# Kernel optimization log

Measured on AMD Instinct MI355X. Metric: run time of the kernel, lower is better.

Reference implementation:

```python
import jax, jax.numpy as jnp
import numpy as np

B, T, D_MODEL, N_HEAD, D_C = 2, 2048, 2048, 16, 512
D_HEAD = D_MODEL // N_HEAD          # 128
D_ROPE = D_C // N_HEAD              # 32 (rope projections are split into heads too)


def setup_inputs() -> dict:
    key = jax.random.key(0)
    ks = jax.random.split(key, 16)
    s = 0.02
    # weights stored as [in, out] (transpose of torch Linear.weight)
    return {
        "x":     jax.random.normal(ks[0], (B, T, D_MODEL), jnp.float32),
        "W_DKV": jax.random.normal(ks[1], (D_MODEL, D_C), jnp.float32) * s,
        "b_DKV": jnp.zeros((D_C,), jnp.float32),
        "W_UK":  jax.random.normal(ks[2], (D_C, D_MODEL), jnp.float32) * s,
        "b_UK":  jnp.zeros((D_MODEL,), jnp.float32),
        "W_UV":  jax.random.normal(ks[3], (D_C, D_MODEL), jnp.float32) * s,
        "b_UV":  jnp.zeros((D_MODEL,), jnp.float32),
        "W_DQ":  jax.random.normal(ks[4], (D_MODEL, D_C), jnp.float32) * s,
        "b_DQ":  jnp.zeros((D_C,), jnp.float32),
        "W_UQ":  jax.random.normal(ks[5], (D_C, D_MODEL), jnp.float32) * s,
        "b_UQ":  jnp.zeros((D_MODEL,), jnp.float32),
        "W_QR":  jax.random.normal(ks[6], (D_C, D_C), jnp.float32) * s,
        "b_QR":  jnp.zeros((D_C,), jnp.float32),
        "W_KR":  jax.random.normal(ks[7], (D_MODEL, D_C), jnp.float32) * s,
        "b_KR":  jnp.zeros((D_C,), jnp.float32),
    }


def _rope(x):
    # x: [B, H, T, d]; matches torch RoPE: split-even/odd then concat halves
    t, d = x.shape[2], x.shape[-1]
    freqs = 10000.0 ** (-(jnp.arange(0, d, 2, dtype=jnp.float32) / d))  # [d/2]
    theta = jnp.arange(t, dtype=jnp.float32)[:, None] * freqs[None, :]  # [T, d/2]
    cos, sin = jnp.cos(theta), jnp.sin(theta)
    x1, x2 = x[..., ::2], x[..., 1::2]
    return jnp.concatenate([x1 * cos - x2 * sin, x1 * sin + x2 * cos], axis=-1)


def _heads(x):
    b, t, _ = x.shape
    return x.reshape(b, t, N_HEAD, -1).transpose(0, 2, 1, 3)  # [B,H,T,dh]


def reference(x, W_DKV, b_DKV, W_UK, b_UK, W_UV, b_UV, W_DQ, b_DQ,
              W_UQ, b_UQ, W_QR, b_QR, W_KR, b_KR):
    b, t, _ = x.shape
    c_kv = x @ W_DKV + b_DKV                 # [B,T,d_c]
    k_content = _heads(c_kv @ W_UK + b_UK)   # [B,H,T,d_head]
    v = _heads(c_kv @ W_UV + b_UV)           # [B,H,T,d_head]
    c_q = x @ W_DQ + b_DQ
    q_content = _heads(c_q @ W_UQ + b_UQ)    # [B,H,T,d_head]
    q_rope = _rope(_heads(c_q @ W_QR + b_QR))  # [B,H,T,d_rope]
    k_rope = _rope(_heads(x @ W_KR + b_KR))    # [B,H,T,d_rope]
    Q = jnp.concatenate([q_content, q_rope], axis=-1)  # [B,H,T,d_head+d_rope]
    K = jnp.concatenate([k_content, k_rope], axis=-1)
    scale = 1.0 / jnp.sqrt(jnp.float32(Q.shape[-1]))
    scores = jnp.einsum("bhqd,bhkd->bhqk", Q, K) * scale
    probs = jax.nn.softmax(scores, axis=-1)
    out = jnp.einsum("bhqk,bhkd->bhqd", probs, v)
    return out.transpose(0, 2, 1, 3).reshape(b, t, -1)
```

## Files before the change

### kernel.cpp

```cpp
#include <hip/hip_runtime.h>
#include <hip/hip_bf16.h>
#include <cstdint>
#include <cstddef>

typedef __attribute__((ext_vector_type(8)))  short bf16x8;
typedef __attribute__((ext_vector_type(4)))  float f32x4;
typedef __attribute__((ext_vector_type(16))) float f32x16;
typedef __attribute__((ext_vector_type(4)))  int   i32x4;

#define DEVINL __device__ __forceinline__

#define ATT_SCALE 0.07905694150420949f
#define QSCALE    (0.07905694150420949f * 1.4426950408889634f)

DEVINL unsigned short f2bf(float f) {
  unsigned int u = __float_as_uint(f);
  u += 0x7fff + ((u >> 16) & 1);
  return (unsigned short)(u >> 16);
}

DEVINL int cvtpk(float lo, float hi) {
  int r;
  asm("v_cvt_pk_bf16_f32 %0, %1, %2" : "=v"(r) : "v"(lo), "v"(hi));
  return r;
}

DEVINL void stage16(const unsigned short* __restrict__ g, unsigned short* lds_u, int lane) {
  (void)lane;
  __builtin_amdgcn_global_load_lds((const __attribute__((address_space(1))) void*)g,
                                   (__attribute__((address_space(3))) void*)lds_u, 16, 0, 0);
}

__global__ void k_cvt_x(const float* __restrict__ x, unsigned short* __restrict__ o, int n) {
  int i = (blockIdx.x * blockDim.x + threadIdx.x) * 4;
  if (i >= n) return;
  float4 v = *reinterpret_cast<const float4*>(x + i);
  ushort4 r;
  r.x = f2bf(v.x); r.y = f2bf(v.y); r.z = f2bf(v.z); r.w = f2bf(v.w);
  *reinterpret_cast<ushort4*>(o + i) = r;
}

struct TwArgs { const float* W[7]; unsigned short* D[7]; };
__global__ void k_tw_all(TwArgs a) {
  __shared__ float t[32][33];
  const int bid = blockIdx.x;
  int w, K, N, bx, by;
  if (bid < 3072)      { w = bid >> 10; int r = bid & 1023; K = 2048; N = 512;  bx = r & 15; by = r >> 4; }
  else if (bid < 6144) { int r = bid - 3072; w = 3 + (r >> 10); r &= 1023; K = 512; N = 2048; bx = r & 63; by = r >> 6; }
  else                 { int r = bid - 6144; w = 6; K = 512; N = 512; bx = r & 15; by = r >> 4; }
  const float* W = a.W[w];
  unsigned short* D = a.D[w];
  const int n0 = bx * 32, k0 = by * 32;
  const int tx = threadIdx.x, ty = threadIdx.y;
#pragma unroll
  for (int j = 0; j < 4; j++)
    t[ty + j * 8][tx] = W[(size_t)(k0 + ty + j * 8) * N + n0 + tx];
  __syncthreads();
#pragma unroll
  for (int j = 0; j < 4; j++)
    D[(size_t)(n0 + ty + j * 8) * K + k0 + tx] = f2bf(t[tx][ty + j * 8]);
}

DEVINL size_t koff(int bh, int t, int d) {
  const int it = t >> 6, t6 = t & 63;
  const int kvt = t6 >> 5, lanelo = t6 & 31;
  const int ks = d >> 4, hi = (d >> 3) & 1, e = d & 7;
  return ((size_t)bh * 32 + it) * 10240 + (size_t)(kvt * 10 + ks) * 512 + (hi * 32 + lanelo) * 8 + e;
}
DEVINL size_t voff(int bh, int t, int dv) {
  const int it = t >> 6, t6 = t & 63;
  const int ks = t6 >> 4, hi = (t6 >> 3) & 1, e = t6 & 7;
  const int dvt = dv >> 5, lanelo = dv & 31;
  return ((size_t)bh * 32 + it) * 8192 + (size_t)(dvt * 4 + ks) * 512 + (hi * 32 + lanelo) * 8 + e;
}

template <int MODE>
__global__ __launch_bounds__(256) void k_gemm(const unsigned short* __restrict__ A,
                                              const unsigned short* __restrict__ BT,
                                              const float* __restrict__ bias0,
                                              const float* __restrict__ bias1,
                                              const float* __restrict__ bias2,
                                              void* __restrict__ o0, void* __restrict__ o1,
                                              void* __restrict__ o2, int K) {
  __shared__ unsigned short sA[128 * 64];
  __shared__ unsigned short sB[128 * 64];
  const int tid = threadIdx.x;
  const int lane = tid & 63, wid = tid >> 6;
  const int wr = wid >> 1, wc = wid & 1;
  const int row0 = blockIdx.y * 128, col0 = blockIdx.x * 128;
  const int lc = lane & 15, lg = lane >> 4;
  const int srow = lane >> 3, scol = (lane & 7) * 8;

  f32x4 acc[4][4];
#pragma unroll
  for (int m = 0; m < 4; m++)
#pragma unroll
    for (int n = 0; n < 4; n++) acc[m][n] = f32x4{0.f, 0.f, 0.f, 0.f};

  for (int k0 = 0; k0 < K; k0 += 64) {
#pragma unroll
    for (int i = 0; i < 4; i++) {
      const int chunk = wid * 4 + i;
      const int r = chunk * 8 + srow;
      stage16(A + (size_t)(row0 + r) * K + k0 + scol, sA + chunk * 512, lane);
      stage16(BT + (size_t)(col0 + r) * K + k0 + scol, sB + chunk * 512, lane);
    }
    asm volatile("s_waitcnt vmcnt(0)" ::: "memory");
    __syncthreads();
#pragma unroll
    for (int ks = 0; ks < 2; ks++) {
      bf16x8 af[4], bfr[4];
#pragma unroll
      for (int m = 0; m < 4; m++)
        af[m] = *reinterpret_cast<const bf16x8*>(sA + (wr * 64 + m * 16 + lc) * 64 + ks * 32 + lg * 8);
#pragma unroll
      for (int n = 0; n < 4; n++)
        bfr[n] = *reinterpret_cast<const bf16x8*>(sB + (wc * 64 + n * 16 + lc) * 64 + ks * 32 + lg * 8);
#pragma unroll
      for (int m = 0; m < 4; m++)
#pragma unroll
        for (int n = 0; n < 4; n++)
          acc[m][n] = __builtin_amdgcn_mfma_f32_16x16x32_bf16(af[m], bfr[n], acc[m][n], 0, 0, 0);
    }
    __syncthreads();
  }

  const int lr = lg * 4;
#pragma unroll
  for (int m = 0; m < 4; m++)
#pragma unroll
    for (int n = 0; n < 4; n++) {
      const int col = col0 + wc * 64 + n * 16 + lc;
      float bv;
      if constexpr (MODE == 10)
        bv = (col < 512) ? bias0[col] : (col < 1024) ? bias1[col - 512] : bias2[col - 1024];
      else
        bv = (col < 2048) ? bias0[col] : bias1[col - 2048];
#pragma unroll
      for (int r = 0; r < 4; r++) {
        const int row = row0 + wr * 64 + m * 16 + lr + r;
        const float v = acc[m][n][r] + bv;
        const int b = row >> 11, t = row & 2047;
        if constexpr (MODE == 10) {
          if (col < 512)        ((unsigned short*)o0)[(size_t)row * 512 + col] = f2bf(v);
          else if (col < 1024)  ((unsigned short*)o1)[(size_t)row * 512 + col - 512] = f2bf(v);
          else                  ((float*)o2)[(size_t)row * 512 + col - 1024] = v;
        } else if constexpr (MODE == 11) {
          if (col < 2048) {
            const int h = col >> 7, d = col & 127;
            ((unsigned short*)o0)[koff(b * 16 + h, t, d)] = f2bf(v);
          } else {
            const int c = col - 2048, h = c >> 7, dv = c & 127;
            ((unsigned short*)o1)[voff(b * 16 + h, t, dv)] = f2bf(v);
          }
        } else {
          if (col < 2048) {
            const int h = col >> 7, d = col & 127;
            ((unsigned short*)o0)[((size_t)(b * 16 + h) * 2048 + t) * 160 + d] = f2bf(v * QSCALE);
          } else {
            ((float*)o1)[(size_t)row * 512 + col - 2048] = v;
          }
        }
      }
    }
}

__global__ void k_rope(const float* __restrict__ qpre, const float* __restrict__ kpre,
                       unsigned short* __restrict__ Qb, unsigned short* __restrict__ Kf) {
  const int idx = blockIdx.x * blockDim.x + threadIdx.x;
  const int which = idx >> 20;
  const int e = idx & 1048575;
  const int i = e & 15, h = (e >> 4) & 15, row = e >> 8;
  const int t = row & 2047, b = row >> 11;
  const float* pre = which ? kpre : qpre;
  const float x1 = pre[(size_t)row * 512 + h * 32 + 2 * i];
  const float x2 = pre[(size_t)row * 512 + h * 32 + 2 * i + 1];
  const float f = exp2f(-(float)i * (13.287712379549449f / 16.f));
  const float th = (float)t * f;
  float sv, cv;
  sincosf(th, &sv, &cv);
  const float o1 = x1 * cv - x2 * sv, o2 = x1 * sv + x2 * cv;
  if (which == 0) {
    const size_t base = ((size_t)(b * 16 + h) * 2048 + t) * 160 + 128;
    Qb[base + i]      = f2bf(o1 * QSCALE);
    Qb[base + 16 + i] = f2bf(o2 * QSCALE);
  } else {
    Kf[koff(b * 16 + h, t, 128 + i)] = f2bf(o1);
    Kf[koff(b * 16 + h, t, 144 + i)] = f2bf(o2);
  }
}

__global__ __launch_bounds__(256, 2) void k_attn(const unsigned short* __restrict__ Qb,
                                                 const unsigned short* __restrict__ Kf,
                                                 const unsigned short* __restrict__ Vf,
                                                 float* __restrict__ out) {
  __shared__ unsigned short sK[2][10240];
  const int lane = threadIdx.x & 63, wid = threadIdx.x >> 6;
  const int lanelo = lane & 31, hi = lane >> 5;

  const int L = blockIdx.x;
  const int xcd = L & 7, w = L >> 3;
  const int bh = xcd * 4 + (w & 3);
  const int qblk = w >> 2;
  const int b = bh >> 4, h = bh & 15;
  const int q0 = qblk * 128 + wid * 32;

  const unsigned short* Qh = Qb + (size_t)bh * 2048 * 160;
  const unsigned short* Kh = Kf + (size_t)bh * 32 * 10240;
  const unsigned short* Vh = Vf + (size_t)bh * 32 * 8192;

  bf16x8 qf[10];
#pragma unroll
  for (int ks = 0; ks < 10; ks++)
    qf[ks] = *reinterpret_cast<const bf16x8*>(Qh + (size_t)(q0 + lanelo) * 160 + ks * 16 + hi * 8);

#pragma unroll
  for (int i = 0; i < 5; i++) {
    const int chunk = wid * 5 + i;
    stage16(Kh + (size_t)chunk * 512 + lane * 8, &sK[0][0] + chunk * 512, lane);
  }

  f32x16 o[4] = {};
  float mrun = -1e30f, lrun = 0.f;

  asm volatile("s_waitcnt vmcnt(0)" ::: "memory");
  __syncthreads();

  int buf = 0;
  for (int it = 0; it < 32; it++) {
    if (it < 31) {
      const unsigned short* src = Kh + (size_t)(it + 1) * 10240;
      unsigned short* dst = &sK[buf ^ 1][0];
#pragma unroll
      for (int i = 0; i < 5; i++) {
        const int chunk = wid * 5 + i;
        stage16(src + (size_t)chunk * 512 + lane * 8, dst + chunk * 512, lane);
      }
    }
    const unsigned short* Vt = Vh + (size_t)it * 8192;
    bf16x8 va[8];
#pragma unroll
    for (int f = 0; f < 8; f++)
      va[f] = *reinterpret_cast<const bf16x8*>(Vt + f * 512 + lane * 8);

    f32x16 s0 = {}, s1 = {};
    const unsigned short* sKb = &sK[buf][0];
#pragma unroll
    for (int ks = 0; ks < 10; ks++) {
      bf16x8 kf0 = *reinterpret_cast<const bf16x8*>(sKb + (size_t)ks * 512 + lane * 8);
      s0 = __builtin_amdgcn_mfma_f32_32x32x16_bf16(kf0, qf[ks], s0, 0, 0, 0);
      bf16x8 kf1 = *reinterpret_cast<const bf16x8*>(sKb + (size_t)(10 + ks) * 512 + lane * 8);
      s1 = __builtin_amdgcn_mfma_f32_32x32x16_bf16(kf1, qf[ks], s1, 0, 0, 0);
    }
    bf16x8 vb[8];
#pragma unroll
    for (int f = 0; f < 8; f++)
      vb[f] = *reinterpret_cast<const bf16x8*>(Vt + (size_t)(8 + f) * 512 + lane * 8);

    float mx = s0[0];
#pragma unroll
    for (int r = 1; r < 16; r++) mx = fmaxf(mx, s0[r]);
#pragma unroll
    for (int r = 0; r < 16; r++) mx = fmaxf(mx, s1[r]);
    mx = fmaxf(mx, __shfl_xor(mx, 32));

    if (__any(mx > mrun + 8.f)) {
      const float mn = fmaxf(mrun, mx);
      const float corr = exp2f(mrun - mn);
      lrun *= corr;
#pragma unroll
      for (int d = 0; d < 4; d++)
#pragma unroll
        for (int r = 0; r < 16; r++) o[d][r] *= corr;
      mrun = mn;
    }

    float pe0[16], pe1[16];
    float rs = 0.f;
#pragma unroll
    for (int r = 0; r < 16; r++) { pe0[r] = exp2f(s0[r] - mrun); rs += pe0[r]; }
#pragma unroll
    for (int r = 0; r < 16; r++) { pe1[r] = exp2f(s1[r] - mrun); rs += pe1[r]; }
    rs += __shfl_xor(rs, 32);
    lrun += rs;

    int W0[8], W1[8], S0w[8], S1w[8];
#pragma unroll
    for (int j = 0; j < 8; j++) {
      W0[j] = cvtpk(pe0[2 * j], pe0[2 * j + 1]);
      W1[j] = cvtpk(pe1[2 * j], pe1[2 * j + 1]);
    }
#pragma unroll
    for (int j = 0; j < 8; j++) {
      S0w[j] = __shfl_xor(W0[j], 32);
      S1w[j] = __shfl_xor(W1[j], 32);
    }
    bf16x8 pa[4];
    {
      i32x4 w0 = hi ? i32x4{S0w[2], S0w[3], W0[2], W0[3]} : i32x4{W0[0], W0[1], S0w[0], S0w[1]};
      i32x4 w1 = hi ? i32x4{S0w[6], S0w[7], W0[6], W0[7]} : i32x4{W0[4], W0[5], S0w[4], S0w[5]};
      i32x4 w2 = hi ? i32x4{S1w[2], S1w[3], W1[2], W1[3]} : i32x4{W1[0], W1[1], S1w[0], S1w[1]};
      i32x4 w3 = hi ? i32x4{S1w[6], S1w[7], W1[6], W1[7]} : i32x4{W1[4], W1[5], S1w[4], S1w[5]};
      pa[0] = __builtin_bit_cast(bf16x8, w0);
      pa[1] = __builtin_bit_cast(bf16x8, w1);
      pa[2] = __builtin_bit_cast(bf16x8, w2);
      pa[3] = __builtin_bit_cast(bf16x8, w3);
    }

#pragma unroll
    for (int ks = 0; ks < 4; ks++) {
      o[0] = __builtin_amdgcn_mfma_f32_32x32x16_bf16(va[ks],     pa[ks], o[0], 0, 0, 0);
      o[1] = __builtin_amdgcn_mfma_f32_32x32x16_bf16(va[4 + ks], pa[ks], o[1], 0, 0, 0);
      o[2] = __builtin_amdgcn_mfma_f32_32x32x16_bf16(vb[ks],     pa[ks], o[2], 0, 0, 0);
      o[3] = __builtin_amdgcn_mfma_f32_32x32x16_bf16(vb[4 + ks], pa[ks], o[3], 0, 0, 0);
    }

    asm volatile("s_waitcnt vmcnt(0)" ::: "memory");
    __syncthreads();
    buf ^= 1;
  }

  const float inv = 1.f / lrun;
  float* sO = reinterpret_cast<float*>(&sK[0][0]) + wid * 1152;
#pragma unroll
  for (int dvt = 0; dvt < 4; dvt++) {
    __syncthreads();
#pragma unroll
    for (int r = 0; r < 16; r++) {
      const int dvl = (r & 3) + 8 * (r >> 2) + 4 * hi;
      sO[lanelo * 36 + dvl] = o[dvt][r] * inv;
    }
    __syncthreads();
#pragma unroll
    for (int p = 0; p < 4; p++) {
      const int q = p * 8 + (lane >> 3), c = (lane & 7) * 4;
      float4 v = *reinterpret_cast<const float4*>(sO + q * 36 + c);
      *reinterpret_cast<float4*>(out + ((size_t)b * 2048 + q0 + q) * 2048 + h * 128 + dvt * 32 + c) = v;
    }
  }
}

extern "C" void kernel_launch(void* const* d_in, const int* in_sizes, int n_in,
                              void* d_out, int out_size, void* d_ws, size_t ws_size,
                              hipStream_t stream) {
  (void)in_sizes; (void)n_in; (void)out_size;
  const float* x     = (const float*)d_in[0];
  const float* W_DKV = (const float*)d_in[1];
  const float* b_DKV = (const float*)d_in[2];
  const float* W_UK  = (const float*)d_in[3];
  const float* b_UK  = (const float*)d_in[4];
  const float* W_UV  = (const float*)d_in[5];
  const float* b_UV  = (const float*)d_in[6];
  const float* W_DQ  = (const float*)d_in[7];
  const float* b_DQ  = (const float*)d_in[8];
  const float* W_UQ  = (const float*)d_in[9];
  const float* b_UQ  = (const float*)d_in[10];
  const float* W_QR  = (const float*)d_in[11];
  const float* b_QR  = (const float*)d_in[12];
  const float* W_KR  = (const float*)d_in[13];
  const float* b_KR  = (const float*)d_in[14];
  float* out = (float*)d_out;

  char* ws = (char*)d_ws;
  unsigned short* xb     = (unsigned short*)(ws + 0);
  unsigned short* WTcat1 = (unsigned short*)(ws + 16777216);
  unsigned short* WTcat2 = (unsigned short*)(ws + 23068672);
  unsigned short* WTcat3 = (unsigned short*)(ws + 27262976);
  unsigned short* ckv    = (unsigned short*)(ws + 29884416);
  unsigned short* cq     = (unsigned short*)(ws + 34078720);
  unsigned short* Qbuf   = (unsigned short*)(ws + 38273024);
  unsigned short* Kfb    = (unsigned short*)(ws + 59244544);
  unsigned short* Vfb    = (unsigned short*)(ws + 80216064);
  float*          qrp    = (float*)(ws + 96993280);
  float*          krp    = (float*)(ws + 105381888);
  if (ws_size < 113770496) return;

  k_cvt_x<<<8192, 256, 0, stream>>>(x, xb, 8388608);

  TwArgs ta;
  ta.W[0] = W_DKV; ta.D[0] = WTcat1;
  ta.W[1] = W_DQ;  ta.D[1] = WTcat1 + (size_t)512 * 2048;
  ta.W[2] = W_KR;  ta.D[2] = WTcat1 + (size_t)1024 * 2048;
  ta.W[3] = W_UK;  ta.D[3] = WTcat2;
  ta.W[4] = W_UV;  ta.D[4] = WTcat2 + (size_t)2048 * 512;
  ta.W[5] = W_UQ;  ta.D[5] = WTcat3;
  ta.W[6] = W_QR;  ta.D[6] = WTcat3 + (size_t)2048 * 512;
  k_tw_all<<<6400, dim3(32, 8), 0, stream>>>(ta);

  k_gemm<10><<<dim3(12, 32), 256, 0, stream>>>(xb, WTcat1, b_DKV, b_DQ, b_KR,
                                               ckv, cq, krp, 2048);
  k_gemm<11><<<dim3(32, 32), 256, 0, stream>>>(ckv, WTcat2, b_UK, b_UV, nullptr,
                                               Kfb, Vfb, nullptr, 512);
  k_gemm<12><<<dim3(20, 32), 256, 0, stream>>>(cq, WTcat3, b_UQ, b_QR, nullptr,
                                               Qbuf, qrp, nullptr, 512);

  k_rope<<<8192, 256, 0, stream>>>(qrp, krp, Qbuf, Kfb);
  k_attn<<<512, 256, 0, stream>>>(Qbuf, Kfb, Vfb, out);
}
```

Measured before the change: 354.3 us.

## Merge up-projection GEMMs into one launch and double-step attention K prefetch

The two K=512 up-projection GEMMs are merged into a single launch with 52 column blocks, so the KV and Q projections run concurrently instead of back to back. The attention loop now processes two K tiles per barrier, using four LDS buffers so each prefetch covers two tiles, and it halves the number of syncs. It also loads all V fragments up front, wraps the MFMA phases in s_setprio, and uses tree reductions for the max and the row sum. LDS per block doubles to about 80KB, which may limit occupancy at two blocks per CU, and holding 16 V fragments raises register pressure.

```diff
diff --git a/kernel.cpp b/kernel.cpp
--- a/kernel.cpp
+++ b/kernel.cpp
@@ -74,16 +74,17 @@
   return ((size_t)bh * 32 + it) * 8192 + (size_t)(dvt * 4 + ks) * 512 + (hi * 32 + lanelo) * 8 + e;
 }
 
-template <int MODE>
-__global__ __launch_bounds__(256) void k_gemm(const unsigned short* __restrict__ A,
-                                              const unsigned short* __restrict__ BT,
-                                              const float* __restrict__ bias0,
-                                              const float* __restrict__ bias1,
-                                              const float* __restrict__ bias2,
-                                              void* __restrict__ o0, void* __restrict__ o1,
-                                              void* __restrict__ o2, int K) {
+__global__ __launch_bounds__(256) void k_gemm1(const unsigned short* __restrict__ A,
+                                               const unsigned short* __restrict__ BT,
+                                               const float* __restrict__ bias0,
+                                               const float* __restrict__ bias1,
+                                               const float* __restrict__ bias2,
+                                               unsigned short* __restrict__ o0,
+                                               unsigned short* __restrict__ o1,
+                                               float* __restrict__ o2) {
   __shared__ unsigned short sA[128 * 64];
   __shared__ unsigned short sB[128 * 64];
+  const int K = 2048;
   const int tid = threadIdx.x;
   const int lane = tid & 63, wid = tid >> 6;
   const int wr = wid >> 1, wc = wid & 1;
@@ -131,34 +132,106 @@
 #pragma unroll
     for (int n = 0; n < 4; n++) {
       const int col = col0 + wc * 64 + n * 16 + lc;
+      const float bv = (col < 512) ? bias0[col] : (col < 1024) ? bias1[col - 512] : bias2[col - 1024];
+#pragma unroll
+      for (int r = 0; r < 4; r++) {
+        const int row = row0 + wr * 64 + m * 16 + lr + r;
+        const float v = acc[m][n][r] + bv;
+        if (col < 512)        o0[(size_t)row * 512 + col] = f2bf(v);
+        else if (col < 1024)  o1[(size_t)row * 512 + col - 512] = f2bf(v);
+        else                  o2[(size_t)row * 512 + col - 1024] = v;
+      }
+    }
+}
+
+__global__ __launch_bounds__(256) void k_gemm2(const unsigned short* __restrict__ ckv,
+                                               const unsigned short* __restrict__ cq,
+                                               const unsigned short* __restrict__ WT2,
+                                               const unsigned short* __restrict__ WT3,
+                                               const float* __restrict__ bUK,
+                                               const float* __restrict__ bUV,
+                                               const float* __restrict__ bUQ,
+                                               const float* __restrict__ bQR,
+                                               unsigned short* __restrict__ Kfb,
+                                               unsigned short* __restrict__ Vfb,
+                                               unsigned short* __restrict__ Qbuf,
+                                               float* __restrict__ qrp) {
+  __shared__ unsigned short sA[128 * 64];
+  __shared__ unsigned short sB[128 * 64];
+  const int K = 512;
+  const bool m11 = blockIdx.x < 32;
+  const unsigned short* A  = m11 ? ckv : cq;
+  const unsigned short* BT = m11 ? WT2 : WT3;
+  const int tid = threadIdx.x;
+  const int lane = tid & 63, wid = tid >> 6;
+  const int wr = wid >> 1, wc = wid & 1;
+  const int row0 = blockIdx.y * 128;
+  const int col0 = (m11 ? blockIdx.x : (blockIdx.x - 32)) * 128;
+  const int lc = lane & 15, lg = lane >> 4;
+  const int srow = lane >> 3, scol = (lane & 7) * 8;
+
+  f32x4 acc[4][4];
+#pragma unroll
+  for (int m = 0; m < 4; m++)
+#pragma unroll
+    for (int n = 0; n < 4; n++) acc[m][n] = f32x4{0.f, 0.f, 0.f, 0.f};
+
+  for (int k0 = 0; k0 < K; k0 += 64) {
+#pragma unroll
+    for (int i = 0; i < 4; i++) {
+      const int chunk = wid * 4 + i;
+      const int r = chunk * 8 + srow;
+      stage16(A + (size_t)(row0 + r) * K + k0 + scol, sA + chunk * 512, lane);
+      stage16(BT + (size_t)(col0 + r) * K + k0 + scol, sB + chunk * 512, lane);
+    }
+    asm volatile("s_waitcnt vmcnt(0)" ::: "memory");
+    __syncthreads();
+#pragma unroll
+    for (int ks = 0; ks < 2; ks++) {
+      bf16x8 af[4], bfr[4];
+#pragma unroll
+      for (int m = 0; m < 4; m++)
+        af[m] = *reinterpret_cast<const bf16x8*>(sA + (wr * 64 + m * 16 + lc) * 64 + ks * 32 + lg * 8);
+#pragma unroll
+      for (int n = 0; n < 4; n++)
+        bfr[n] = *reinterpret_cast<const bf16x8*>(sB + (wc * 64 + n * 16 + lc) * 64 + ks * 32 + lg * 8);
+#pragma unroll
+      for (int m = 0; m < 4; m++)
+#pragma unroll
+        for (int n = 0; n < 4; n++)
+          acc[m][n] = __builtin_amdgcn_mfma_f32_16x16x32_bf16(af[m], bfr[n], acc[m][n], 0, 0, 0);
+    }
+    __syncthreads();
+  }
+
+  const int lr = lg * 4;
+#pragma unroll
+  for (int m = 0; m < 4; m++)
+#pragma unroll
+    for (int n = 0; n < 4; n++) {
+      const int col = col0 + wc * 64 + n * 16 + lc;
       float bv;
-      if constexpr (MODE == 10)
-        bv = (col < 512) ? bias0[col] : (col < 1024) ? bias1[col - 512] : bias2[col - 1024];
-      else
-        bv = (col < 2048) ? bias0[col] : bias1[col - 2048];
+      if (m11) bv = (col < 2048) ? bUK[col] : bUV[col - 2048];
+      else     bv = (col < 2048) ? bUQ[col] : bQR[col - 2048];
 #pragma unroll
       for (int r = 0; r < 4; r++) {
         const int row = row0 + wr * 64 + m * 16 + lr + r;
         const float v = acc[m][n][r] + bv;
         const int b = row >> 11, t = row & 2047;
-        if constexpr (MODE == 10) {
-          if (col < 512)        ((unsigned short*)o0)[(size_t)row * 512 + col] = f2bf(v);
-          else if (col < 1024)  ((unsigned short*)o1)[(size_t)row * 512 + col - 512] = f2bf(v);
-          else                  ((float*)o2)[(size_t)row * 512 + col - 1024] = v;
-        } else if constexpr (MODE == 11) {
+        if (m11) {
           if (col < 2048) {
             const int h = col >> 7, d = col & 127;
-            ((unsigned short*)o0)[koff(b * 16 + h, t, d)] = f2bf(v);
+            Kfb[koff(b * 16 + h, t, d)] = f2bf(v);
           } else {
             const int c = col - 2048, h = c >> 7, dv = c & 127;
-            ((unsigned short*)o1)[voff(b * 16 + h, t, dv)] = f2bf(v);
+            Vfb[voff(b * 16 + h, t, dv)] = f2bf(v);
           }
         } else {
           if (col < 2048) {
             const int h = col >> 7, d = col & 127;
-            ((unsigned short*)o0)[((size_t)(b * 16 + h) * 2048 + t) * 160 + d] = f2bf(v * QSCALE);
+            Qbuf[((size_t)(b * 16 + h) * 2048 + t) * 160 + d] = f2bf(v * QSCALE);
           } else {
-            ((float*)o1)[(size_t)row * 512 + col - 2048] = v;
+            qrp[(size_t)row * 512 + col - 2048] = v;
           }
         }
       }
@@ -190,11 +263,109 @@
   }
 }
 
+DEVINL float vmax32(const f32x16& a, const f32x16& b) {
+  float t[16];
+#pragma unroll
+  for (int j = 0; j < 16; j++) t[j] = fmaxf(a[j], b[j]);
+#pragma unroll
+  for (int s = 8; s >= 1; s >>= 1)
+#pragma unroll
+    for (int j = 0; j < s; j++) t[j] = fmaxf(t[j], t[j + s]);
+  return t[0];
+}
+
+DEVINL void loadV(const unsigned short* __restrict__ Vt, bf16x8 v[16], int lane) {
+#pragma unroll
+  for (int f = 0; f < 16; f++)
+    v[f] = *reinterpret_cast<const bf16x8*>(Vt + (size_t)f * 512 + lane * 8);
+}
+
+DEVINL void subiter(const unsigned short* __restrict__ sKb, const bf16x8 qf[10],
+                    const bf16x8 vfr[16], f32x16 o[4], float& mrun, float& lrun,
+                    int lane, int hi) {
+  f32x16 s0 = {}, s1 = {};
+  __builtin_amdgcn_s_setprio(1);
+#pragma unroll
+  for (int ks = 0; ks < 10; ks++) {
+    bf16x8 kf0 = *reinterpret_cast<const bf16x8*>(sKb + (size_t)ks * 512 + lane * 8);
+    s0 = __builtin_amdgcn_mfma_f32_32x32x16_bf16(kf0, qf[ks], s0, 0, 0, 0);
+    bf16x8 kf1 = *reinterpret_cast<const bf16x8*>(sKb + (size_t)(10 + ks) * 512 + lane * 8);
+    s1 = __builtin_amdgcn_mfma_f32_32x32x16_bf16(kf1, qf[ks], s1, 0, 0, 0);
+  }
+  __builtin_amdgcn_s_setprio(0);
+
+  float mx = vmax32(s0, s1);
+  mx = fmaxf(mx, __shfl_xor(mx, 32));
+
+  if (__any(mx > mrun + 8.f)) {
+    const float mn = fmaxf(mrun, mx);
+    const float corr = exp2f(mrun - mn);
+    lrun *= corr;
+#pragma unroll
+    for (int d = 0; d < 4; d++)
+#pragma unroll
+      for (int r = 0; r < 16; r++) o[d][r] *= corr;
+    mrun = mn;
+  }
+
+  float pe0[16], pe1[16];
+#pragma unroll
+  for (int r = 0; r < 16; r++) pe0[r] = exp2f(s0[r] - mrun);
+#pragma unroll
+  for (int r = 0; r < 16; r++) pe1[r] = exp2f(s1[r] - mrun);
+  float a[16];
+#pragma unroll
+  for (int j = 0; j < 8; j++) {
+    a[j]     = pe0[2 * j] + pe0[2 * j + 1];
+    a[8 + j] = pe1[2 * j] + pe1[2 * j + 1];
+  }
+#pragma unroll
+  for (int s = 8; s >= 1; s >>= 1)
+#pragma unroll
+    for (int j = 0; j < s; j++) a[j] += a[j + s];
+  float rs = a[0];
+  rs += __shfl_xor(rs, 32);
+  lrun += rs;
+
+  int W0[8], W1[8], S0w[8], S1w[8];
+#pragma unroll
+  for (int j = 0; j < 8; j++) {
+    W0[j] = cvtpk(pe0[2 * j], pe0[2 * j + 1]);
+    W1[j] = cvtpk(pe1[2 * j], pe1[2 * j + 1]);
+  }
+#pragma unroll
+  for (int j = 0; j < 8; j++) {
+    S0w[j] = __shfl_xor(W0[j], 32);
+    S1w[j] = __shfl_xor(W1[j], 32);
+  }
+  bf16x8 pa[4];
+  {
+    i32x4 w0 = hi ? i32x4{S0w[2], S0w[3], W0[2], W0[3]} : i32x4{W0[0], W0[1], S0w[0], S0w[1]};
+    i32x4 w1 = hi ? i32x4{S0w[6], S0w[7], W0[6], W0[7]} : i32x4{W0[4], W0[5], S0w[4], S0w[5]};
+    i32x4 w2 = hi ? i32x4{S1w[2], S1w[3], W1[2], W1[3]} : i32x4{W1[0], W1[1], S1w[0], S1w[1]};
+    i32x4 w3 = hi ? i32x4{S1w[6], S1w[7], W1[6], W1[7]} : i32x4{W1[4], W1[5], S1w[4], S1w[5]};
+    pa[0] = __builtin_bit_cast(bf16x8, w0);
+    pa[1] = __builtin_bit_cast(bf16x8, w1);
+    pa[2] = __builtin_bit_cast(bf16x8, w2);
+    pa[3] = __builtin_bit_cast(bf16x8, w3);
+  }
+
+  __builtin_amdgcn_s_setprio(1);
+#pragma unroll
+  for (int ks = 0; ks < 4; ks++) {
+    o[0] = __builtin_amdgcn_mfma_f32_32x32x16_bf16(vfr[ks],      pa[ks], o[0], 0, 0, 0);
+    o[1] = __builtin_amdgcn_mfma_f32_32x32x16_bf16(vfr[4 + ks],  pa[ks], o[1], 0, 0, 0);
+    o[2] = __builtin_amdgcn_mfma_f32_32x32x16_bf16(vfr[8 + ks],  pa[ks], o[2], 0, 0, 0);
+    o[3] = __builtin_amdgcn_mfma_f32_32x32x16_bf16(vfr[12 + ks], pa[ks], o[3], 0, 0, 0);
+  }
+  __builtin_amdgcn_s_setprio(0);
+}
+
 __global__ __launch_bounds__(256, 2) void k_attn(const unsigned short* __restrict__ Qb,
                                                  const unsigned short* __restrict__ Kf,
                                                  const unsigned short* __restrict__ Vf,
                                                  float* __restrict__ out) {
-  __shared__ unsigned short sK[2][10240];
+  __shared__ unsigned short sK[4][10240];
   const int lane = threadIdx.x & 63, wid = threadIdx.x >> 6;
   const int lanelo = lane & 31, hi = lane >> 5;
 
@@ -215,8 +386,8 @@
     qf[ks] = *reinterpret_cast<const bf16x8*>(Qh + (size_t)(q0 + lanelo) * 160 + ks * 16 + hi * 8);
 
 #pragma unroll
-  for (int i = 0; i < 5; i++) {
-    const int chunk = wid * 5 + i;
+  for (int i = 0; i < 10; i++) {
+    const int chunk = wid * 10 + i;
     stage16(Kh + (size_t)chunk * 512 + lane * 8, &sK[0][0] + chunk * 512, lane);
   }
 
@@ -226,98 +397,26 @@
   asm volatile("s_waitcnt vmcnt(0)" ::: "memory");
   __syncthreads();
 
-  int buf = 0;
-  for (int it = 0; it < 32; it++) {
-    if (it < 31) {
-      const unsigned short* src = Kh + (size_t)(it + 1) * 10240;
-      unsigned short* dst = &sK[buf ^ 1][0];
-#pragma unroll
-      for (int i = 0; i < 5; i++) {
-        const int chunk = wid * 5 + i;
+  for (int p = 0; p < 16; p++) {
+    const int base = (p & 1) * 2;
+    bf16x8 vA[16];
+    loadV(Vh + (size_t)(2 * p) * 8192, vA, lane);
+    if (p < 15) {
+      const unsigned short* src = Kh + (size_t)(2 * p + 2) * 10240;
+      unsigned short* dst = &sK[base ^ 2][0];
+#pragma unroll
+      for (int i = 0; i < 10; i++) {
+        const int chunk = wid * 10 + i;
         stage16(src + (size_t)chunk * 512 + lane * 8, dst + chunk * 512, lane);
       }
     }
-    const unsigned short* Vt = Vh + (size_t)it * 8192;
-    bf16x8 va[8];
-#pragma unroll
-    for (int f = 0; f < 8; f++)
-      va[f] = *reinterpret_cast<const bf16x8*>(Vt + f * 512 + lane * 8);
-
-    f32x16 s0 = {}, s1 = {};
-    const unsigned short* sKb = &sK[buf][0];
-#pragma unroll
-    for (int ks = 0; ks < 10; ks++) {
-      bf16x8 kf0 = *reinterpret_cast<const bf16x8*>(sKb + (size_t)ks * 512 + lane * 8);
-      s0 = __builtin_amdgcn_mfma_f32_32x32x16_bf16(kf0, qf[ks], s0, 0, 0, 0);
-      bf16x8 kf1 = *reinterpret_cast<const bf16x8*>(sKb + (size_t)(10 + ks) * 512 + lane * 8);
-      s1 = __builtin_amdgcn_mfma_f32_32x32x16_bf16(kf1, qf[ks], s1, 0, 0, 0);
-    }
-    bf16x8 vb[8];
-#pragma unroll
-    for (int f = 0; f < 8; f++)
-      vb[f] = *reinterpret_cast<const bf16x8*>(Vt + (size_t)(8 + f) * 512 + lane * 8);
-
-    float mx = s0[0];
-#pragma unroll
-    for (int r = 1; r < 16; r++) mx = fmaxf(mx, s0[r]);
-#pragma unroll
-    for (int r = 0; r < 16; r++) mx = fmaxf(mx, s1[r]);
-    mx = fmaxf(mx, __shfl_xor(mx, 32));
-
-    if (__any(mx > mrun + 8.f)) {
-      const float mn = fmaxf(mrun, mx);
-      const float corr = exp2f(mrun - mn);
-      lrun *= corr;
-#pragma unroll
-      for (int d = 0; d < 4; d++)
-#pragma unroll
-        for (int r = 0; r < 16; r++) o[d][r] *= corr;
-      mrun = mn;
-    }
-
-    float pe0[16], pe1[16];
-    float rs = 0.f;
-#pragma unroll
-    for (int r = 0; r < 16; r++) { pe0[r] = exp2f(s0[r] - mrun); rs += pe0[r]; }
-#pragma unroll
-    for (int r = 0; r < 16; r++) { pe1[r] = exp2f(s1[r] - mrun); rs += pe1[r]; }
-    rs += __shfl_xor(rs, 32);
-    lrun += rs;
-
-    int W0[8], W1[8], S0w[8], S1w[8];
-#pragma unroll
-    for (int j = 0; j < 8; j++) {
-      W0[j] = cvtpk(pe0[2 * j], pe0[2 * j + 1]);
-      W1[j] = cvtpk(pe1[2 * j], pe1[2 * j + 1]);
-    }
-#pragma unroll
-    for (int j = 0; j < 8; j++) {
-      S0w[j] = __shfl_xor(W0[j], 32);
-      S1w[j] = __shfl_xor(W1[j], 32);
-    }
-    bf16x8 pa[4];
-    {
-      i32x4 w0 = hi ? i32x4{S0w[2], S0w[3], W0[2], W0[3]} : i32x4{W0[0], W0[1], S0w[0], S0w[1]};
-      i32x4 w1 = hi ? i32x4{S0w[6], S0w[7], W0[6], W0[7]} : i32x4{W0[4], W0[5], S0w[4], S0w[5]};
-      i32x4 w2 = hi ? i32x4{S1w[2], S1w[3], W1[2], W1[3]} : i32x4{W1[0], W1[1], S1w[0], S1w[1]};
-      i32x4 w3 = hi ? i32x4{S1w[6], S1w[7], W1[6], W1[7]} : i32x4{W1[4], W1[5], S1w[4], S1w[5]};
-      pa[0] = __builtin_bit_cast(bf16x8, w0);
-      pa[1] = __builtin_bit_cast(bf16x8, w1);
-      pa[2] = __builtin_bit_cast(bf16x8, w2);
-      pa[3] = __builtin_bit_cast(bf16x8, w3);
-    }
-
-#pragma unroll
-    for (int ks = 0; ks < 4; ks++) {
-      o[0] = __builtin_amdgcn_mfma_f32_32x32x16_bf16(va[ks],     pa[ks], o[0], 0, 0, 0);
-      o[1] = __builtin_amdgcn_mfma_f32_32x32x16_bf16(va[4 + ks], pa[ks], o[1], 0, 0, 0);
-      o[2] = __builtin_amdgcn_mfma_f32_32x32x16_bf16(vb[ks],     pa[ks], o[2], 0, 0, 0);
-      o[3] = __builtin_amdgcn_mfma_f32_32x32x16_bf16(vb[4 + ks], pa[ks], o[3], 0, 0, 0);
-    }
+    subiter(&sK[base][0], qf, vA, o, mrun, lrun, lane, hi);
+    bf16x8 vB[16];
+    loadV(Vh + (size_t)(2 * p + 1) * 8192, vB, lane);
+    subiter(&sK[base + 1][0], qf, vB, o, mrun, lrun, lane, hi);
 
     asm volatile("s_waitcnt vmcnt(0)" ::: "memory");
     __syncthreads();
-    buf ^= 1;
   }
 
   const float inv = 1.f / lrun;
@@ -387,12 +486,10 @@
   ta.W[6] = W_QR;  ta.D[6] = WTcat3 + (size_t)2048 * 512;
   k_tw_all<<<6400, dim3(32, 8), 0, stream>>>(ta);
 
-  k_gemm<10><<<dim3(12, 32), 256, 0, stream>>>(xb, WTcat1, b_DKV, b_DQ, b_KR,
-                                               ckv, cq, krp, 2048);
-  k_gemm<11><<<dim3(32, 32), 256, 0, stream>>>(ckv, WTcat2, b_UK, b_UV, nullptr,
-                                               Kfb, Vfb, nullptr, 512);
-  k_gemm<12><<<dim3(20, 32), 256, 0, stream>>>(cq, WTcat3, b_UQ, b_QR, nullptr,
-                                               Qbuf, qrp, nullptr, 512);
+  k_gemm1<<<dim3(12, 32), 256, 0, stream>>>(xb, WTcat1, b_DKV, b_DQ, b_KR, ckv, cq, krp);
+  k_gemm2<<<dim3(52, 32), 256, 0, stream>>>(ckv, cq, WTcat2, WTcat3,
+                                            b_UK, b_UV, b_UQ, b_QR,
+                                            Kfb, Vfb, Qbuf, qrp);
 
   k_rope<<<8192, 256, 0, stream>>>(qrp, krp, Qbuf, Kfb);
   k_attn<<<512, 256, 0, stream>>>(Qbuf, Kfb, Vfb, out);
```

New measurement: 370.7 us. +4.6%, slower.
